# Kernel optimization log

Hardware: AMD Instinct MI355X
Metric: run time of the kernel (lower is better)

Reference implementation:

```python
import jax, jax.numpy as jnp
import numpy as np

B, T, D = 4, 1024, 1024
H, S = 16, 64            # n_heads, stalk_dim
HID = 3072               # int(D*3.0), already even
P_ADIC_BASE, P_ADIC_MAX = 2, 16


def quant6(w):
    # per-tensor symmetric 6-bit fake-quant (abs-max scale, round, clamp)
    scale = jnp.abs(w).max() / 31.0 + 1e-8
    return jnp.clip(jnp.round(w / scale), -31, 31) * scale


def q6_ste(w):
    # straight-through estimator: identity gradient
    return w + jax.lax.stop_gradient(quant6(w) - w)


def layernorm(x, g, b, eps=1e-5):
    mu = x.mean(-1, keepdims=True)
    var = ((x - mu) ** 2).mean(-1, keepdims=True)
    return (x - mu) * jax.lax.rsqrt(var + eps) * g + b


def build_p_adic_bias(t, p=P_ADIC_BASE, max_val=P_ADIC_MAX):
    idx = np.arange(t)
    d = np.abs(idx[:, None] - idx[None, :])
    nz = d > 0
    vp = np.zeros_like(d)
    work = d.copy()
    while True:
        div = nz & (work % p == 0)
        if not div.any():
            break
        vp = vp + div.astype(vp.dtype)
        work = np.where(div, work // p, work)
    vals = np.minimum(vp, max_val).astype(np.float32)
    vals = np.where(nz, vals, np.float32(max_val))
    return jnp.asarray(vals / max_val)


def setup_inputs() -> dict:
    key = jax.random.key(0)
    ks = jax.random.split(key, 12)
    sd_d = 1.0 / np.sqrt(D)
    sd_s = 1.0 / np.sqrt(S)
    sd_h = 1.0 / np.sqrt(HID)
    return {
        "x": jax.random.normal(ks[0], (B, T, D), jnp.float32),
        "wq": jax.random.normal(ks[1], (D, D), jnp.float32) * sd_d,
        "wk": jax.random.normal(ks[2], (D, D), jnp.float32) * sd_d,
        "wv": jax.random.normal(ks[3], (D, D), jnp.float32) * sd_d,
        "wo": jax.random.normal(ks[4], (D, D), jnp.float32) * sd_d,
        "su": jax.random.normal(ks[5], (S, S), jnp.float32) * sd_s,
        "sv": jax.random.normal(ks[6], (S, S), jnp.float32) * sd_s,
        "p_scale": jnp.ones((1,), jnp.float32) * 0.1,
        "norm1_g": jnp.ones((D,), jnp.float32),
        "norm1_b": jnp.zeros((D,), jnp.float32),
        "norm2_g": jnp.ones((D,), jnp.float32),
        "norm2_b": jnp.zeros((D,), jnp.float32),
        "w_up": jax.random.normal(ks[7], (HID, D), jnp.float32) * sd_d,
        "w_down": jax.random.normal(ks[8], (D, HID), jnp.float32) * sd_h,
        "theta": jnp.zeros((HID // 2,), jnp.float32),
        "mlp_norm_g": jnp.ones((HID,), jnp.float32),
        "mlp_norm_b": jnp.zeros((HID,), jnp.float32),
    }


def _sheaf_attention(xn, wq, wk, wv, wo, su, sv, p_scale):
    # projections with inline 6-bit fake-quant of weights
    Q = (xn @ q6_ste(wq).T).reshape(B, T, H, S).transpose(0, 2, 1, 3)  # [B,H,T,S]
    K = (xn @ q6_ste(wk).T).reshape(B, T, H, S).transpose(0, 2, 1, 3)
    V = (xn @ q6_ste(wv).T).reshape(B, T, H, S).transpose(0, 2, 1, 3)
    Qs = Q @ q6_ste(su).T   # stalk map on head dim
    Ks = K @ q6_ste(sv).T
    scale = 1.0 / np.sqrt(S)
    scores = jnp.einsum('bhts,bhus->bhtu', Qs, Ks) * scale
    p_bias = build_p_adic_bias(T)                     # [T,T], constant
    scores = scores + p_scale[0] * p_bias[None, None]
    causal = jnp.triu(jnp.ones((T, T), bool), k=1)
    scores = jnp.where(causal[None, None], -jnp.inf, scores)
    attn = jax.nn.softmax(scores, axis=-1)
    out = jnp.einsum('bhtu,bhus->bhts', attn, V)
    out = out.transpose(0, 2, 1, 3).reshape(B, T, D)
    return out @ q6_ste(wo).T


def _so2_mlp(xn, w_up, w_down, theta, ng, nb):
    h = xn @ q6_ste(w_up).T                          # [B,T,HID]
    hp = h.reshape(B, T, HID // 2, 2)
    a, b = hp[..., 0], hp[..., 1]
    c, s = jnp.cos(theta), jnp.sin(theta)            # [HID/2]
    rot = jnp.stack([c * a - s * b, s * a + c * b], axis=-1).reshape(B, T, HID)
    rot = layernorm(rot, ng, nb)
    rot = jax.nn.silu(rot)
    return rot @ q6_ste(w_down).T


def reference(x, wq, wk, wv, wo, su, sv, p_scale, norm1_g, norm1_b,
              norm2_g, norm2_b, w_up, w_down, theta, mlp_norm_g, mlp_norm_b):
    # pre-norm residual block: x = x + attn(ln1(x)); x = x + mlp(ln2(x))
    x = x + _sheaf_attention(layernorm(x, norm1_g, norm1_b),
                             wq, wk, wv, wo, su, sv, p_scale)
    x = x + _so2_mlp(layernorm(x, norm2_g, norm2_b),
                     w_up, w_down, theta, mlp_norm_g, mlp_norm_b)
    return x
```

## Files before the change

kernel.cpp:

```cpp
#include <hip/hip_runtime.h>
#include <stdint.h>

typedef __bf16 bf16;
typedef __attribute__((ext_vector_type(8))) __bf16 bf16x8;
typedef __attribute__((ext_vector_type(4))) __bf16 bf16x4;
typedef __attribute__((ext_vector_type(2))) __bf16 bf16x2;
typedef __attribute__((ext_vector_type(4))) float f32x4;

#define GLOBAL_AS __attribute__((address_space(1)))
#define LDS_AS __attribute__((address_space(3)))

static __device__ __forceinline__ bf16 f2bf(float f) {
  unsigned u = __builtin_bit_cast(unsigned, f);
  u += 0x7fffu + ((u >> 16) & 1u);
  unsigned short h = (unsigned short)(u >> 16);
  return __builtin_bit_cast(bf16, h);
}

static __device__ __forceinline__ float waveSum(float v) {
  #pragma unroll
  for (int o = 32; o > 0; o >>= 1) v += __shfl_xor(v, o);
  return v;
}
static __device__ __forceinline__ float waveMax(float v) {
  #pragma unroll
  for (int o = 32; o > 0; o >>= 1) v = fmaxf(v, __shfl_xor(v, o));
  return v;
}

static __device__ __forceinline__ int swz(int r, int c) { return c ^ ((r >> 1) & 3); }

struct QTask { const float* src; bf16* dst; int n; int slot; int blk0; };
struct QTasks { QTask t[8]; };

__global__ __launch_bounds__(256) void absmax_all(QTasks qt, unsigned* amax) {
  int ti = 0;
  #pragma unroll
  for (int i = 1; i < 8; ++i) if ((int)blockIdx.x >= qt.t[i].blk0) ti = i;
  const QTask tk = qt.t[ti];
  const int base = (blockIdx.x - tk.blk0) * 4096;
  const float4* s4 = (const float4*)(tk.src + base);
  float m = 0.f;
  #pragma unroll
  for (int i = 0; i < 4; ++i) {
    float4 w = s4[i * 256 + threadIdx.x];
    m = fmaxf(m, fmaxf(fmaxf(fabsf(w.x), fabsf(w.y)), fmaxf(fabsf(w.z), fabsf(w.w))));
  }
  m = waveMax(m);
  __shared__ float red[4];
  if ((threadIdx.x & 63) == 0) red[threadIdx.x >> 6] = m;
  __syncthreads();
  if (threadIdx.x == 0) {
    float mm = fmaxf(fmaxf(red[0], red[1]), fmaxf(red[2], red[3]));
    atomicMax(amax + tk.slot, __float_as_uint(mm));
  }
}

__global__ __launch_bounds__(256) void quant_all(QTasks qt, const unsigned* amax) {
  int ti = 0;
  #pragma unroll
  for (int i = 1; i < 8; ++i) if ((int)blockIdx.x >= qt.t[i].blk0) ti = i;
  const QTask tk = qt.t[ti];
  const float scale = __uint_as_float(amax[tk.slot]) / 31.0f + 1e-8f;
  const int base = (blockIdx.x - tk.blk0) * 4096;
  const float4* s4 = (const float4*)(tk.src + base);
  bf16x4* d4 = (bf16x4*)(tk.dst + base);
  #pragma unroll
  for (int i = 0; i < 4; ++i) {
    float4 w = s4[i * 256 + threadIdx.x];
    bf16x4 o;
    float q;
    q = fminf(31.f, fmaxf(-31.f, rintf(w.x / scale))); o[0] = f2bf(q * scale);
    q = fminf(31.f, fmaxf(-31.f, rintf(w.y / scale))); o[1] = f2bf(q * scale);
    q = fminf(31.f, fmaxf(-31.f, rintf(w.z / scale))); o[2] = f2bf(q * scale);
    q = fminf(31.f, fmaxf(-31.f, rintf(w.w / scale))); o[3] = f2bf(q * scale);
    d4[i * 256 + threadIdx.x] = o;
  }
}

__global__ __launch_bounds__(256) void premul_stalk(const bf16* __restrict__ Su,
                                                    const bf16* __restrict__ Sv,
                                                    const bf16* __restrict__ Wqk,
                                                    bf16* __restrict__ Wdst) {
  const int tensor = blockIdx.x >> 4;
  const int h = blockIdx.x & 15;
  const int c0 = blockIdx.y * 64;
  const bf16* S = tensor ? Sv : Su;
  const bf16* W = Wqk + (size_t)tensor * 1024 * 1024 + (size_t)h * 64 * 1024;
  bf16* D = Wdst + (size_t)tensor * 1024 * 1024 + (size_t)h * 64 * 1024;
  const int tid = threadIdx.x;
  const int i = tid >> 2;
  const int c = c0 + (tid & 3) * 16;
  bf16x8 srow[8];
  #pragma unroll
  for (int k = 0; k < 8; ++k) srow[k] = *(const bf16x8*)(S + i * 64 + k * 8);
  float acc[16] = {};
  #pragma unroll
  for (int j = 0; j < 64; ++j) {
    const float s = (float)srow[j >> 3][j & 7];
    const bf16x8 w0 = *(const bf16x8*)(W + (size_t)j * 1024 + c);
    const bf16x8 w1 = *(const bf16x8*)(W + (size_t)j * 1024 + c + 8);
    #pragma unroll
    for (int k = 0; k < 8; ++k) { acc[k] += s * (float)w0[k]; acc[8 + k] += s * (float)w1[k]; }
  }
  bf16x8 o0, o1;
  #pragma unroll
  for (int k = 0; k < 8; ++k) { o0[k] = f2bf(acc[k]); o1[k] = f2bf(acc[8 + k]); }
  *(bf16x8*)(D + (size_t)i * 1024 + c) = o0;
  *(bf16x8*)(D + (size_t)i * 1024 + c + 8) = o1;
}

__global__ __launch_bounds__(256) void ln_kernel(const float* __restrict__ x,
                                                 const float* __restrict__ g,
                                                 const float* __restrict__ b,
                                                 bf16* __restrict__ out) {
  const int row = blockIdx.x, tid = threadIdx.x;
  const float4 v = ((const float4*)(x + (size_t)row * 1024))[tid];
  float s = v.x + v.y + v.z + v.w;
  float ss = v.x * v.x + v.y * v.y + v.z * v.z + v.w * v.w;
  s = waveSum(s); ss = waveSum(ss);
  __shared__ float rs[4], rq[4];
  if ((tid & 63) == 0) { rs[tid >> 6] = s; rq[tid >> 6] = ss; }
  __syncthreads();
  s = rs[0] + rs[1] + rs[2] + rs[3];
  ss = rq[0] + rq[1] + rq[2] + rq[3];
  const float mu = s * (1.f / 1024.f);
  const float var = ss * (1.f / 1024.f) - mu * mu;
  const float rstd = rsqrtf(var + 1e-5f);
  const float4 gv = ((const float4*)g)[tid];
  const float4 bv = ((const float4*)b)[tid];
  bf16x4 o;
  o[0] = f2bf((v.x - mu) * rstd * gv.x + bv.x);
  o[1] = f2bf((v.y - mu) * rstd * gv.y + bv.y);
  o[2] = f2bf((v.z - mu) * rstd * gv.z + bv.z);
  o[3] = f2bf((v.w - mu) * rstd * gv.w + bv.w);
  ((bf16x4*)(out + (size_t)row * 1024))[tid] = o;
}

template <int EPI>
__global__ __launch_bounds__(256) void gemm_bt(const bf16* __restrict__ A,
                                               const bf16* __restrict__ B,
                                               bf16* __restrict__ C,
                                               bf16* __restrict__ Qsb,
                                               bf16* __restrict__ Ksb,
                                               bf16* __restrict__ Vtg,
                                               int M, int N, int K) {
  constexpr int BM = 128, BN = 128, BK = 32;
  __shared__ bf16 As[BM * BK];
  __shared__ bf16 Bs[BN * BK];
  const int tid = threadIdx.x;
  const int wave = tid >> 6, lane = tid & 63, quad = lane >> 4, l16 = lane & 15;
  const int bm0 = blockIdx.y * BM, bn0 = blockIdx.x * BN;
  const int wr = (wave >> 1) * 64, wc = (wave & 1) * 64;
  f32x4 acc[4][4] = {};

  for (int k0 = 0; k0 < K; k0 += BK) {
    __syncthreads();
    #pragma unroll
    for (int i = 0; i < 2; ++i) {
      const int id = tid + i * 256;
      const int r = id >> 2, c = swz(r, id & 3) * 8;
      __builtin_amdgcn_global_load_lds(
          (GLOBAL_AS void*)(A + (size_t)(bm0 + r) * K + k0 + c),
          (LDS_AS void*)(As + (size_t)(i * 256 + wave * 64) * 8), 16, 0, 0);
      __builtin_amdgcn_global_load_lds(
          (GLOBAL_AS void*)(B + (size_t)(bn0 + r) * K + k0 + c),
          (LDS_AS void*)(Bs + (size_t)(i * 256 + wave * 64) * 8), 16, 0, 0);
    }
    __syncthreads();
    bf16x8 af[4], bfr[4];
    #pragma unroll
    for (int mi = 0; mi < 4; ++mi) {
      const int r = wr + mi * 16 + l16;
      af[mi] = *(const bf16x8*)(As + (r * 4 + swz(r, quad)) * 8);
    }
    #pragma unroll
    for (int ni = 0; ni < 4; ++ni) {
      const int r = wc + ni * 16 + l16;
      bfr[ni] = *(const bf16x8*)(Bs + (r * 4 + swz(r, quad)) * 8);
    }
    #pragma unroll
    for (int mi = 0; mi < 4; ++mi)
      #pragma unroll
      for (int ni = 0; ni < 4; ++ni)
        acc[mi][ni] = __builtin_amdgcn_mfma_f32_16x16x32_bf16(af[mi], bfr[ni], acc[mi][ni], 0, 0, 0);
  }

  #pragma unroll
  for (int ni = 0; ni < 4; ++ni) {
    const int col = bn0 + wc + ni * 16 + l16;
    if constexpr (EPI == 0) {
      #pragma unroll
      for (int mi = 0; mi < 4; ++mi)
        #pragma unroll
        for (int reg = 0; reg < 4; ++reg) {
          const int row = bm0 + wr + mi * 16 + quad * 4 + reg;
          C[(size_t)row * N + col] = f2bf(acc[mi][ni][reg]);
        }
    } else {
      if (col < 2048) {
        const int h = (col >> 6) & 15, s = col & 63;
        bf16* dst = (col < 1024 ? Qsb : Ksb) + (size_t)h * 1024 * 64 + s;
        #pragma unroll
        for (int mi = 0; mi < 4; ++mi)
          #pragma unroll
          for (int reg = 0; reg < 4; ++reg) {
            const int row = bm0 + wr + mi * 16 + quad * 4 + reg;
            const int b = row >> 10, t = row & 1023;
            dst[((size_t)b * 16 * 1024 + t) * 64] = f2bf(acc[mi][ni][reg]);
          }
      } else {
        const int h = (col >> 6) & 15, s = col & 63;
        const int bq = bm0 >> 10;
        bf16* vdst = Vtg + (((size_t)(bq * 16 + h) * 64 + s) * 1024) + (bm0 & 1023) + wr + quad * 4;
        #pragma unroll
        for (int mi = 0; mi < 4; ++mi) {
          bf16x4 vv;
          #pragma unroll
          for (int reg = 0; reg < 4; ++reg) vv[reg] = f2bf(acc[mi][ni][reg]);
          *(bf16x4*)(vdst + mi * 16) = vv;
        }
      }
    }
  }
}

__global__ __launch_bounds__(256) void gemm_bt_split(const bf16* __restrict__ A,
                                                     const bf16* __restrict__ B,
                                                     bf16* __restrict__ P,
                                                     int M, int N, int Kfull, int Kper) {
  constexpr int BM = 128, BN = 128, BK = 32;
  __shared__ bf16 As[BM * BK];
  __shared__ bf16 Bs[BN * BK];
  const int tid = threadIdx.x;
  const int wave = tid >> 6, lane = tid & 63, quad = lane >> 4, l16 = lane & 15;
  const int lin = blockIdx.x + 8 * blockIdx.y;
  const int xcd = lin & 7, idx = lin >> 3;
  const int bm0 = (xcd * 4 + (idx & 3)) * BM;
  const int bn0 = (idx >> 2) * BN;
  const int wr = (wave >> 1) * 64, wc = (wave & 1) * 64;
  const int kbeg = blockIdx.z * Kper;
  const int kend = min(kbeg + Kper, Kfull);
  bf16* Pz = P + (size_t)blockIdx.z * M * N;
  f32x4 acc[4][4] = {};

  for (int k0 = kbeg; k0 < kend; k0 += BK) {
    __syncthreads();
    #pragma unroll
    for (int i = 0; i < 2; ++i) {
      const int id = tid + i * 256;
      const int r = id >> 2, c = swz(r, id & 3) * 8;
      __builtin_amdgcn_global_load_lds(
          (GLOBAL_AS void*)(A + (size_t)(bm0 + r) * Kfull + k0 + c),
          (LDS_AS void*)(As + (size_t)(i * 256 + wave * 64) * 8), 16, 0, 0);
      __builtin_amdgcn_global_load_lds(
          (GLOBAL_AS void*)(B + (size_t)(bn0 + r) * Kfull + k0 + c),
          (LDS_AS void*)(Bs + (size_t)(i * 256 + wave * 64) * 8), 16, 0, 0);
    }
    __syncthreads();
    bf16x8 af[4], bfr[4];
    #pragma unroll
    for (int mi = 0; mi < 4; ++mi) {
      const int r = wr + mi * 16 + l16;
      af[mi] = *(const bf16x8*)(As + (r * 4 + swz(r, quad)) * 8);
    }
    #pragma unroll
    for (int ni = 0; ni < 4; ++ni) {
      const int r = wc + ni * 16 + l16;
      bfr[ni] = *(const bf16x8*)(Bs + (r * 4 + swz(r, quad)) * 8);
    }
    #pragma unroll
    for (int mi = 0; mi < 4; ++mi)
      #pragma unroll
      for (int ni = 0; ni < 4; ++ni)
        acc[mi][ni] = __builtin_amdgcn_mfma_f32_16x16x32_bf16(af[mi], bfr[ni], acc[mi][ni], 0, 0, 0);
  }

  #pragma unroll
  for (int mi = 0; mi < 4; ++mi)
    #pragma unroll
    for (int ni = 0; ni < 4; ++ni)
      #pragma unroll
      for (int reg = 0; reg < 4; ++reg) {
        const int row = bm0 + wr + mi * 16 + quad * 4 + reg;
        const int col = bn0 + wc + ni * 16 + l16;
        Pz[(size_t)row * N + col] = f2bf(acc[mi][ni][reg]);
      }
}

__global__ __launch_bounds__(256) void reduce_wo_ln(const float* __restrict__ x,
                                                    const bf16* __restrict__ P,
                                                    const float* __restrict__ g,
                                                    const float* __restrict__ b,
                                                    float* __restrict__ y,
                                                    bf16* __restrict__ lnout) {
  constexpr size_t MN = (size_t)4096 * 1024;
  const int row = blockIdx.x, tid = threadIdx.x;
  const size_t base = (size_t)row * 1024;
  const float4 vx = ((const float4*)(x + base))[tid];
  const bf16x4 p0 = ((const bf16x4*)(P + base))[tid];
  const bf16x4 p1 = ((const bf16x4*)(P + base + MN))[tid];
  const bf16x4 p2 = ((const bf16x4*)(P + base + 2 * MN))[tid];
  float4 v;
  v.x = vx.x + (float)p0[0] + (float)p1[0] + (float)p2[0];
  v.y = vx.y + (float)p0[1] + (float)p1[1] + (float)p2[1];
  v.z = vx.z + (float)p0[2] + (float)p1[2] + (float)p2[2];
  v.w = vx.w + (float)p0[3] + (float)p1[3] + (float)p2[3];
  ((float4*)(y + base))[tid] = v;
  float s = v.x + v.y + v.z + v.w;
  float ss = v.x * v.x + v.y * v.y + v.z * v.z + v.w * v.w;
  s = waveSum(s); ss = waveSum(ss);
  __shared__ float rs[4], rq[4];
  if ((tid & 63) == 0) { rs[tid >> 6] = s; rq[tid >> 6] = ss; }
  __syncthreads();
  s = rs[0] + rs[1] + rs[2] + rs[3];
  ss = rq[0] + rq[1] + rq[2] + rq[3];
  const float mu = s * (1.f / 1024.f);
  const float var = ss * (1.f / 1024.f) - mu * mu;
  const float rstd = rsqrtf(var + 1e-5f);
  const float4 gv = ((const float4*)g)[tid];
  const float4 bv = ((const float4*)b)[tid];
  bf16x4 o;
  o[0] = f2bf((v.x - mu) * rstd * gv.x + bv.x);
  o[1] = f2bf((v.y - mu) * rstd * gv.y + bv.y);
  o[2] = f2bf((v.z - mu) * rstd * gv.z + bv.z);
  o[3] = f2bf((v.w - mu) * rstd * gv.w + bv.w);
  ((bf16x4*)(lnout + base))[tid] = o;
}

__global__ __launch_bounds__(256) void reduce_down(float* __restrict__ y,
                                                   const bf16* __restrict__ P) {
  constexpr size_t MN = (size_t)4096 * 1024;
  const size_t i = (size_t)blockIdx.x * 256 + threadIdx.x;
  const float4 vy = ((const float4*)y)[i];
  const bf16x4 p0 = ((const bf16x4*)P)[i];
  const bf16x4 p1 = ((const bf16x4*)(P + MN))[i];
  const bf16x4 p2 = ((const bf16x4*)(P + 2 * MN))[i];
  float4 v;
  v.x = vy.x + (float)p0[0] + (float)p1[0] + (float)p2[0];
  v.y = vy.y + (float)p0[1] + (float)p1[1] + (float)p2[1];
  v.z = vy.z + (float)p0[2] + (float)p1[2] + (float)p2[2];
  v.w = vy.w + (float)p0[3] + (float)p1[3] + (float)p2[3];
  ((float4*)y)[i] = v;
}

__global__ __launch_bounds__(256) void attn_flash(const bf16* __restrict__ Qs,
                                                  const bf16* __restrict__ Ks,
                                                  const bf16* __restrict__ Vtg,
                                                  const float* __restrict__ p_scale_ptr,
                                                  bf16* __restrict__ out) {
  constexpr int LDP = 72;
  const int bh = blockIdx.x;
  const int b = bh >> 4, h = bh & 15;
  const int ttile = 15 - (int)blockIdx.y;
  const int t0 = ttile * 64;
  const int tid = threadIdx.x, wave = tid >> 6, lane = tid & 63, quad = lane >> 4, l16 = lane & 15;

  __shared__ bf16 Kst[64 * LDP];
  __shared__ bf16 Vt[64 * LDP];
  __shared__ bf16 Plds[4][16 * LDP];

  const float pscale2 = p_scale_ptr[0] * 1.44269504f;
  const float sc2 = 0.125f * 1.44269504f;

  const bf16* Qb = Qs + ((size_t)bh * 1024 + t0) * 64;
  const bf16* Kb = Ks + ((size_t)bh * 1024) * 64;
  const bf16* Vb = Vtg + ((size_t)bh * 64) * 1024;

  const int trow = wave * 16 + l16;
  const bf16x8 qf0 = *(const bf16x8*)(Qb + trow * 64 + quad * 8);
  const bf16x8 qf1 = *(const bf16x8*)(Qb + trow * 64 + 32 + quad * 8);

  float lsum[4] = {0.f, 0.f, 0.f, 0.f};
  f32x4 Oacc[4] = {};

  bf16x8 st[4];
  auto loadTile = [&](int u0) {
    #pragma unroll
    for (int i = 0; i < 2; ++i) {
      const int cid = tid + i * 256;
      st[i] = *(const bf16x8*)(Kb + (size_t)u0 * 64 + cid * 8);
      st[2 + i] = *(const bf16x8*)(Vb + (size_t)(cid >> 3) * 1024 + u0 + (cid & 7) * 8);
    }
  };
  loadTile(0);

  for (int ut = 0; ut <= ttile; ++ut) {
    const int u0 = ut * 64;
    #pragma unroll
    for (int i = 0; i < 2; ++i) {
      const int cid = tid + i * 256;
      const int r = cid >> 3, c8 = (cid & 7) * 8;
      *(bf16x8*)(Kst + r * LDP + c8) = st[i];
      *(bf16x8*)(Vt + r * LDP + c8) = st[2 + i];
    }
    __syncthreads();
    if (ut < ttile) loadTile(u0 + 64);

    f32x4 sc[4];
    #pragma unroll
    for (int ni = 0; ni < 4; ++ni) {
      const bf16x8 k0 = *(const bf16x8*)(Kst + (ni * 16 + l16) * LDP + quad * 8);
      const bf16x8 k1 = *(const bf16x8*)(Kst + (ni * 16 + l16) * LDP + 32 + quad * 8);
      f32x4 z = {};
      z = __builtin_amdgcn_mfma_f32_16x16x32_bf16(qf0, k0, z, 0, 0, 0);
      z = __builtin_amdgcn_mfma_f32_16x16x32_bf16(qf1, k1, z, 0, 0, 0);
      sc[ni] = z;
    }
    const bool diag = (ut == ttile);
    #pragma unroll
    for (int reg = 0; reg < 4; ++reg) {
      const int t = t0 + wave * 16 + quad * 4 + reg;
      #pragma unroll
      for (int ni = 0; ni < 4; ++ni) {
        const int u = u0 + ni * 16 + l16;
        const int d = t - u;
        float v = sc[ni][reg] * sc2;
        if (diag && d < 0) {
          v = -1e30f;
        } else {
          const float bias = (d == 0) ? 1.0f : (float)__builtin_ctz(d) * 0.0625f;
          v += pscale2 * bias;
        }
        const float p = exp2f(fminf(v, 80.f) - 8.f);
        lsum[reg] += p;
        Plds[wave][(quad * 4 + reg) * LDP + ni * 16 + l16] = f2bf(p);
      }
    }
    const bf16x8 pf0 = *(const bf16x8*)(&Plds[wave][l16 * LDP + quad * 8]);
    const bf16x8 pf1 = *(const bf16x8*)(&Plds[wave][l16 * LDP + 32 + quad * 8]);
    #pragma unroll
    for (int ni = 0; ni < 4; ++ni) {
      const bf16x8 v0 = *(const bf16x8*)(Vt + (ni * 16 + l16) * LDP + quad * 8);
      const bf16x8 v1 = *(const bf16x8*)(Vt + (ni * 16 + l16) * LDP + 32 + quad * 8);
      Oacc[ni] = __builtin_amdgcn_mfma_f32_16x16x32_bf16(pf0, v0, Oacc[ni], 0, 0, 0);
      Oacc[ni] = __builtin_amdgcn_mfma_f32_16x16x32_bf16(pf1, v1, Oacc[ni], 0, 0, 0);
    }
    __syncthreads();
  }

  #pragma unroll
  for (int reg = 0; reg < 4; ++reg) {
    float rs = lsum[reg];
    #pragma unroll
    for (int o = 1; o < 16; o <<= 1) rs += __shfl_xor(rs, o);
    lsum[reg] = 1.0f / rs;
  }

  #pragma unroll
  for (int ni = 0; ni < 4; ++ni)
    #pragma unroll
    for (int reg = 0; reg < 4; ++reg) {
      const int t = t0 + wave * 16 + quad * 4 + reg;
      out[((size_t)(b * 1024 + t)) * 1024 + h * 64 + ni * 16 + l16] = f2bf(Oacc[ni][reg] * lsum[reg]);
    }
}

__global__ __launch_bounds__(256) void rot_ln_silu(const bf16* __restrict__ hb,
                                                   const float* __restrict__ theta,
                                                   const float* __restrict__ g,
                                                   const float* __restrict__ bb,
                                                   bf16* __restrict__ out) {
  const int row = blockIdx.x, tid = threadIdx.x;
  const bf16* hr = hb + (size_t)row * 3072;
  float r[12];
  float s = 0.f, ss = 0.f;
  #pragma unroll
  for (int i = 0; i < 6; ++i) {
    const int p = tid + i * 256;
    const bf16x2 ab = *(const bf16x2*)(hr + 2 * p);
    const float a = (float)ab[0], b_ = (float)ab[1];
    const float th = theta[p];
    const float c = cosf(th), sn = sinf(th);
    const float r0 = c * a - sn * b_;
    const float r1 = sn * a + c * b_;
    r[2 * i] = r0; r[2 * i + 1] = r1;
    s += r0 + r1;
    ss += r0 * r0 + r1 * r1;
  }
  s = waveSum(s); ss = waveSum(ss);
  __shared__ float rs_[4], rq_[4];
  if ((tid & 63) == 0) { rs_[tid >> 6] = s; rq_[tid >> 6] = ss; }
  __syncthreads();
  s = rs_[0] + rs_[1] + rs_[2] + rs_[3];
  ss = rq_[0] + rq_[1] + rq_[2] + rq_[3];
  const float mu = s * (1.f / 3072.f);
  const float var = ss * (1.f / 3072.f) - mu * mu;
  const float rstd = rsqrtf(var + 1e-5f);
  bf16* orow = out + (size_t)row * 3072;
  #pragma unroll
  for (int i = 0; i < 6; ++i) {
    const int p = tid + i * 256;
    const float2 gv = *(const float2*)(g + 2 * p);
    const float2 bv = *(const float2*)(bb + 2 * p);
    const float y0 = (r[2 * i] - mu) * rstd * gv.x + bv.x;
    const float y1 = (r[2 * i + 1] - mu) * rstd * gv.y + bv.y;
    const float o0 = y0 / (1.f + expf(-y0));
    const float o1 = y1 / (1.f + expf(-y1));
    bf16x2 o; o[0] = f2bf(o0); o[1] = f2bf(o1);
    *(bf16x2*)(orow + 2 * p) = o;
  }
}

extern "C" void kernel_launch(void* const* d_in, const int* in_sizes, int n_in,
                              void* d_out, int out_size, void* d_ws, size_t ws_size,
                              hipStream_t stream) {
  const float* x    = (const float*)d_in[0];
  const float* wq   = (const float*)d_in[1];
  const float* wk   = (const float*)d_in[2];
  const float* wv   = (const float*)d_in[3];
  const float* wo   = (const float*)d_in[4];
  const float* su   = (const float*)d_in[5];
  const float* sv   = (const float*)d_in[6];
  const float* psc  = (const float*)d_in[7];
  const float* n1g  = (const float*)d_in[8];
  const float* n1b  = (const float*)d_in[9];
  const float* n2g  = (const float*)d_in[10];
  const float* n2b  = (const float*)d_in[11];
  const float* wup  = (const float*)d_in[12];
  const float* wdn  = (const float*)d_in[13];
  const float* th   = (const float*)d_in[14];
  const float* mg   = (const float*)d_in[15];
  const float* mb   = (const float*)d_in[16];
  float* outp = (float*)d_out;

  char* ws = (char*)d_ws;
  size_t off = 0;
  auto alloc = [&](size_t bytes) { size_t o = off; off += (bytes + 255) & ~(size_t)255; return o; };
  constexpr size_t MB84 = (size_t)4096 * 1024 * 2;
  unsigned* amax = (unsigned*)(ws + alloc(32));
  bf16* Su    = (bf16*)(ws + alloc(4096 * 2));
  bf16* Sv    = (bf16*)(ws + alloc(4096 * 2));
  bf16* Wo    = (bf16*)(ws + alloc((size_t)1024 * 1024 * 2));
  bf16* Wup   = (bf16*)(ws + alloc((size_t)3072 * 1024 * 2));
  bf16* Wdn   = (bf16*)(ws + alloc((size_t)1024 * 3072 * 2));
  bf16* Wqkv2 = (bf16*)(ws + alloc((size_t)3072 * 1024 * 2));
  bf16* Wqk   = (bf16*)(ws + alloc((size_t)2048 * 1024 * 2));
  bf16* lnbuf = (bf16*)(ws + alloc(MB84));
  char* arena = ws + alloc(6 * MB84);
  bf16* Qsb   = (bf16*)(arena);
  bf16* Ksb   = (bf16*)(arena + MB84);
  bf16* Vtg   = (bf16*)(arena + 2 * MB84);
  bf16* attno = (bf16*)(arena + 3 * MB84);
  bf16* hbuf  = (bf16*)(arena);
  bf16* gbuf  = (bf16*)(arena + 3 * MB84);
  bf16* Pbuf  = (bf16*)(ws + alloc((size_t)3 * 4096 * 1024 * 2));

  hipMemsetAsync(amax, 0, 32, stream);

  QTasks qt;
  int blk = 0;
  auto add = [&](int i, const float* s, bf16* d, int n) {
    qt.t[i].src = s; qt.t[i].dst = d; qt.t[i].n = n; qt.t[i].slot = i; qt.t[i].blk0 = blk;
    blk += n / 4096;
  };
  add(0, wq, Wqk, 1024 * 1024);
  add(1, wk, Wqk + (size_t)1024 * 1024, 1024 * 1024);
  add(2, wv, Wqkv2 + (size_t)2048 * 1024, 1024 * 1024);
  add(3, wo, Wo, 1024 * 1024);
  add(4, su, Su, 4096);
  add(5, sv, Sv, 4096);
  add(6, wup, Wup, 3072 * 1024);
  add(7, wdn, Wdn, 3072 * 1024);

  absmax_all<<<blk, 256, 0, stream>>>(qt, amax);
  quant_all<<<blk, 256, 0, stream>>>(qt, amax);
  premul_stalk<<<dim3(32, 16), 256, 0, stream>>>(Su, Sv, Wqk, Wqkv2);

  ln_kernel<<<4096, 256, 0, stream>>>(x, n1g, n1b, lnbuf);
  gemm_bt<1><<<dim3(24, 32), 256, 0, stream>>>(lnbuf, Wqkv2, nullptr, Qsb, Ksb, Vtg, 4096, 3072, 1024);
  attn_flash<<<dim3(64, 16), 256, 0, stream>>>(Qsb, Ksb, Vtg, psc, attno);
  gemm_bt_split<<<dim3(8, 32, 3), 256, 0, stream>>>(attno, Wo, Pbuf, 4096, 1024, 1024, 352);
  reduce_wo_ln<<<4096, 256, 0, stream>>>(x, Pbuf, n2g, n2b, outp, lnbuf);
  gemm_bt<0><<<dim3(24, 32), 256, 0, stream>>>(lnbuf, Wup, hbuf, nullptr, nullptr, nullptr, 4096, 3072, 1024);
  rot_ln_silu<<<4096, 256, 0, stream>>>(hbuf, th, mg, mb, gbuf);
  gemm_bt_split<<<dim3(8, 32, 3), 256, 0, stream>>>(gbuf, Wdn, Pbuf, 4096, 1024, 3072, 1024);
  reduce_down<<<4096, 256, 0, stream>>>(outp, Pbuf);
}
```

Baseline: 378.0 us.

## Process two 64-row query tiles per attention block to reuse K/V tiles

Each attention block now handles 128 query rows as two 64-row halves that share each K/V tile loaded into LDS, which halves the grid along the query dimension. K and V fragments are read into registers once per tile and used by both halves, and the first half skips tiles that lie entirely above its causal diagonal. This is meant to cut global and LDS traffic for K/V. The cost is more registers per thread, fewer blocks (512 instead of 1024), and a less even causal workload across blocks.

```diff
diff --git a/kernel.cpp b/kernel.cpp
--- a/kernel.cpp
+++ b/kernel.cpp
@@ -352,8 +352,8 @@
   constexpr int LDP = 72;
   const int bh = blockIdx.x;
   const int b = bh >> 4, h = bh & 15;
-  const int ttile = 15 - (int)blockIdx.y;
-  const int t0 = ttile * 64;
+  const int qt = 7 - (int)blockIdx.y;
+  const int t0 = qt * 128;
   const int tid = threadIdx.x, wave = tid >> 6, lane = tid & 63, quad = lane >> 4, l16 = lane & 15;
 
   __shared__ bf16 Kst[64 * LDP];
@@ -368,11 +368,13 @@
   const bf16* Vb = Vtg + ((size_t)bh * 64) * 1024;
 
   const int trow = wave * 16 + l16;
-  const bf16x8 qf0 = *(const bf16x8*)(Qb + trow * 64 + quad * 8);
-  const bf16x8 qf1 = *(const bf16x8*)(Qb + trow * 64 + 32 + quad * 8);
-
-  float lsum[4] = {0.f, 0.f, 0.f, 0.f};
-  f32x4 Oacc[4] = {};
+  const bf16x8 qA0 = *(const bf16x8*)(Qb + trow * 64 + quad * 8);
+  const bf16x8 qA1 = *(const bf16x8*)(Qb + trow * 64 + 32 + quad * 8);
+  const bf16x8 qB0 = *(const bf16x8*)(Qb + (64 + trow) * 64 + quad * 8);
+  const bf16x8 qB1 = *(const bf16x8*)(Qb + (64 + trow) * 64 + 32 + quad * 8);
+
+  float lsumA[4] = {0.f, 0.f, 0.f, 0.f}, lsumB[4] = {0.f, 0.f, 0.f, 0.f};
+  f32x4 OA[4] = {}, OB[4] = {};
 
   bf16x8 st[4];
   auto loadTile = [&](int u0) {
@@ -385,7 +387,8 @@
   };
   loadTile(0);
 
-  for (int ut = 0; ut <= ttile; ++ut) {
+  const int utmax = 2 * qt + 1;
+  for (int ut = 0; ut <= utmax; ++ut) {
     const int u0 = ut * 64;
     #pragma unroll
     for (int i = 0; i < 2; ++i) {
@@ -395,64 +398,81 @@
       *(bf16x8*)(Vt + r * LDP + c8) = st[2 + i];
     }
     __syncthreads();
-    if (ut < ttile) loadTile(u0 + 64);
-
-    f32x4 sc[4];
+    if (ut < utmax) loadTile(u0 + 64);
+
+    bf16x8 k0[4], k1[4], v0[4], v1[4];
     #pragma unroll
     for (int ni = 0; ni < 4; ++ni) {
-      const bf16x8 k0 = *(const bf16x8*)(Kst + (ni * 16 + l16) * LDP + quad * 8);
-      const bf16x8 k1 = *(const bf16x8*)(Kst + (ni * 16 + l16) * LDP + 32 + quad * 8);
-      f32x4 z = {};
-      z = __builtin_amdgcn_mfma_f32_16x16x32_bf16(qf0, k0, z, 0, 0, 0);
-      z = __builtin_amdgcn_mfma_f32_16x16x32_bf16(qf1, k1, z, 0, 0, 0);
-      sc[ni] = z;
-    }
-    const bool diag = (ut == ttile);
+      k0[ni] = *(const bf16x8*)(Kst + (ni * 16 + l16) * LDP + quad * 8);
+      k1[ni] = *(const bf16x8*)(Kst + (ni * 16 + l16) * LDP + 32 + quad * 8);
+      v0[ni] = *(const bf16x8*)(Vt + (ni * 16 + l16) * LDP + quad * 8);
+      v1[ni] = *(const bf16x8*)(Vt + (ni * 16 + l16) * LDP + 32 + quad * 8);
+    }
+
+    #pragma unroll
+    for (int half = 0; half < 2; ++half) {
+      const int tbase = t0 + half * 64;
+      if (u0 > tbase + 63) continue;
+      const bf16x8 q0 = half ? qB0 : qA0;
+      const bf16x8 q1 = half ? qB1 : qA1;
+      float* lsum = half ? lsumB : lsumA;
+      f32x4* Oacc = half ? OB : OA;
+      const bool diag = (u0 + 63 >= tbase);
+
+      f32x4 sc[4];
+      #pragma unroll
+      for (int ni = 0; ni < 4; ++ni) {
+        f32x4 z = {};
+        z = __builtin_amdgcn_mfma_f32_16x16x32_bf16(q0, k0[ni], z, 0, 0, 0);
+        z = __builtin_amdgcn_mfma_f32_16x16x32_bf16(q1, k1[ni], z, 0, 0, 0);
+        sc[ni] = z;
+      }
+      #pragma unroll
+      for (int reg = 0; reg < 4; ++reg) {
+        const int t = tbase + wave * 16 + quad * 4 + reg;
+        #pragma unroll
+        for (int ni = 0; ni < 4; ++ni) {
+          const int u = u0 + ni * 16 + l16;
+          const int d = t - u;
+          float v = sc[ni][reg] * sc2;
+          if (diag && d < 0) {
+            v = -1e30f;
+          } else {
+            const float bias = (d == 0) ? 1.0f : (float)__builtin_ctz(d) * 0.0625f;
+            v += pscale2 * bias;
+          }
+          const float p = exp2f(fminf(v, 80.f) - 8.f);
+          lsum[reg] += p;
+          Plds[wave][(quad * 4 + reg) * LDP + ni * 16 + l16] = f2bf(p);
+        }
+      }
+      const bf16x8 pf0 = *(const bf16x8*)(&Plds[wave][l16 * LDP + quad * 8]);
+      const bf16x8 pf1 = *(const bf16x8*)(&Plds[wave][l16 * LDP + 32 + quad * 8]);
+      #pragma unroll
+      for (int ni = 0; ni < 4; ++ni) {
+        Oacc[ni] = __builtin_amdgcn_mfma_f32_16x16x32_bf16(pf0, v0[ni], Oacc[ni], 0, 0, 0);
+        Oacc[ni] = __builtin_amdgcn_mfma_f32_16x16x32_bf16(pf1, v1[ni], Oacc[ni], 0, 0, 0);
+      }
+    }
+    __syncthreads();
+  }
+
+  #pragma unroll
+  for (int reg = 0; reg < 4; ++reg) {
+    float ra = lsumA[reg], rb = lsumB[reg];
+    #pragma unroll
+    for (int o = 1; o < 16; o <<= 1) { ra += __shfl_xor(ra, o); rb += __shfl_xor(rb, o); }
+    lsumA[reg] = 1.0f / ra;
+    lsumB[reg] = 1.0f / rb;
+  }
+
+  #pragma unroll
+  for (int ni = 0; ni < 4; ++ni)
     #pragma unroll
     for (int reg = 0; reg < 4; ++reg) {
-      const int t = t0 + wave * 16 + quad * 4 + reg;
-      #pragma unroll
-      for (int ni = 0; ni < 4; ++ni) {
-        const int u = u0 + ni * 16 + l16;
-        const int d = t - u;
-        float v = sc[ni][reg] * sc2;
-        if (diag && d < 0) {
-          v = -1e30f;
-        } else {
-          const float bias = (d == 0) ? 1.0f : (float)__builtin_ctz(d) * 0.0625f;
-          v += pscale2 * bias;
-        }
-        const float p = exp2f(fminf(v, 80.f) - 8.f);
-        lsum[reg] += p;
-        Plds[wave][(quad * 4 + reg) * LDP + ni * 16 + l16] = f2bf(p);
-      }
-    }
-    const bf16x8 pf0 = *(const bf16x8*)(&Plds[wave][l16 * LDP + quad * 8]);
-    const bf16x8 pf1 = *(const bf16x8*)(&Plds[wave][l16 * LDP + 32 + quad * 8]);
-    #pragma unroll
-    for (int ni = 0; ni < 4; ++ni) {
-      const bf16x8 v0 = *(const bf16x8*)(Vt + (ni * 16 + l16) * LDP + quad * 8);
-      const bf16x8 v1 = *(const bf16x8*)(Vt + (ni * 16 + l16) * LDP + 32 + quad * 8);
-      Oacc[ni] = __builtin_amdgcn_mfma_f32_16x16x32_bf16(pf0, v0, Oacc[ni], 0, 0, 0);
-      Oacc[ni] = __builtin_amdgcn_mfma_f32_16x16x32_bf16(pf1, v1, Oacc[ni], 0, 0, 0);
-    }
-    __syncthreads();
-  }
-
-  #pragma unroll
-  for (int reg = 0; reg < 4; ++reg) {
-    float rs = lsum[reg];
-    #pragma unroll
-    for (int o = 1; o < 16; o <<= 1) rs += __shfl_xor(rs, o);
-    lsum[reg] = 1.0f / rs;
-  }
-
-  #pragma unroll
-  for (int ni = 0; ni < 4; ++ni)
-    #pragma unroll
-    for (int reg = 0; reg < 4; ++reg) {
-      const int t = t0 + wave * 16 + quad * 4 + reg;
-      out[((size_t)(b * 1024 + t)) * 1024 + h * 64 + ni * 16 + l16] = f2bf(Oacc[ni][reg] * lsum[reg]);
+      const int tA = t0 + wave * 16 + quad * 4 + reg;
+      out[((size_t)(b * 1024 + tA)) * 1024 + h * 64 + ni * 16 + l16] = f2bf(OA[ni][reg] * lsumA[reg]);
+      out[((size_t)(b * 1024 + tA + 64)) * 1024 + h * 64 + ni * 16 + l16] = f2bf(OB[ni][reg] * lsumB[reg]);
     }
 }
 
@@ -569,7 +589,7 @@
 
   ln_kernel<<<4096, 256, 0, stream>>>(x, n1g, n1b, lnbuf);
   gemm_bt<1><<<dim3(24, 32), 256, 0, stream>>>(lnbuf, Wqkv2, nullptr, Qsb, Ksb, Vtg, 4096, 3072, 1024);
-  attn_flash<<<dim3(64, 16), 256, 0, stream>>>(Qsb, Ksb, Vtg, psc, attno);
+  attn_flash<<<dim3(64, 8), 256, 0, stream>>>(Qsb, Ksb, Vtg, psc, attno);
   gemm_bt_split<<<dim3(8, 32, 3), 256, 0, stream>>>(attno, Wo, Pbuf, 4096, 1024, 1024, 352);
   reduce_wo_ln<<<4096, 256, 0, stream>>>(x, Pbuf, n2g, n2b, outp, lnbuf);
   gemm_bt<0><<<dim3(24, 32), 256, 0, stream>>>(lnbuf, Wup, hbuf, nullptr, nullptr, nullptr, 4096, 3072, 1024);
```

Result: slower. 393.6 us (+4.1%).
